# Performance work log

Hardware: AMD Instinct MI355X
Metric: run time of the kernel (lower is better)

The kernel has to match this reference:

```python
import jax, jax.numpy as jnp
import numpy as np

N_NODES = 100000
N_EDGES = 1000000
S = 64      # n_hidden_scalars
F = 64      # n_hidden_edge_feats
RBF = 16    # rbf_dim
V = 16      # n_vec_channels
IN_DIM = 2 * S + F + RBF  # 208, EdgeUpdate MLP input


def _layernorm(x, g, b):
    m = x.mean(-1, keepdims=True)
    var = ((x - m) ** 2).mean(-1, keepdims=True)
    return (x - m) / jnp.sqrt(var + 1e-5) * g + b


def _gvp(s, v, Wh, Wu, Ws, bs, sigmoid_gate):
    # s: [N, S]; v: [N, v_in, 3]
    vh = jnp.einsum('nvc,vh->nhc', v, Wh)          # [N, h, 3]
    vu = jnp.einsum('nhc,hu->nuc', vh, Wu)          # [N, v_out, 3]
    sh = jnp.sqrt(jnp.sum(vh * vh, axis=-1) + 1e-8)  # [N, h]
    s_out = jax.nn.silu(jnp.concatenate([s, sh], axis=-1) @ Ws + bs)
    vn = jnp.sqrt(jnp.sum(vu * vu, axis=-1, keepdims=True) + 1e-8)  # [N, v_out, 1]
    gate = jax.nn.sigmoid(vn) if sigmoid_gate else vn
    return s_out, gate * vu


def setup_inputs() -> dict:
    key = jax.random.key(0)
    ks = jax.random.split(key, 24)

    def nrm(k, shape, fan_in):
        return jax.random.normal(k, shape, dtype=jnp.float32) / np.sqrt(fan_in)

    inp = {
        'node_scalars': jax.random.normal(ks[0], (N_NODES, S), dtype=jnp.float32),
        'positions': jax.random.normal(ks[1], (N_NODES, 3), dtype=jnp.float32),
        'vectors': jax.random.normal(ks[2], (N_NODES, V, 3), dtype=jnp.float32),
        'edge_feats': jax.random.normal(ks[3], (N_EDGES, F), dtype=jnp.float32),
        'd': jax.random.uniform(ks[4], (N_EDGES, RBF), dtype=jnp.float32),
        'src_idx': jax.random.randint(ks[5], (N_EDGES,), 0, N_NODES, dtype=jnp.int32),
        'dst_idx': jax.random.randint(ks[6], (N_EDGES,), 0, N_NODES, dtype=jnp.int32),
        # EdgeUpdate MLP + LayerNorm params
        'W1': nrm(ks[7], (IN_DIM, F), IN_DIM), 'b1': jnp.zeros((F,), jnp.float32),
        'W2': nrm(ks[8], (F, F), F),           'b2': jnp.zeros((F,), jnp.float32),
        'ln_g': jnp.ones((F,), jnp.float32),   'ln_b': jnp.zeros((F,), jnp.float32),
        # GVP 0: s 64->64, v 16->16 (h=16), sigmoid vector gate
        'gvp0_Wh': nrm(ks[9], (V, V), V), 'gvp0_Wu': nrm(ks[10], (V, V), V),
        'gvp0_Ws': nrm(ks[11], (S + V, S), S + V), 'gvp0_bs': jnp.zeros((S,), jnp.float32),
        # GVP 1: same shapes
        'gvp1_Wh': nrm(ks[12], (V, V), V), 'gvp1_Wu': nrm(ks[13], (V, V), V),
        'gvp1_Ws': nrm(ks[14], (S + V, S), S + V), 'gvp1_bs': jnp.zeros((S,), jnp.float32),
        # GVP 2 (last): v 16->1, identity vector activation
        'gvp2_Wh': nrm(ks[15], (V, V), V), 'gvp2_Wu': nrm(ks[16], (V, 1), V),
        'gvp2_Ws': nrm(ks[17], (S + V, S), S + V), 'gvp2_bs': jnp.zeros((S,), jnp.float32),
    }
    return inp


def reference(node_scalars, positions, vectors, edge_feats, d, src_idx, dst_idx,
              W1, b1, W2, b2, ln_g, ln_b,
              gvp0_Wh, gvp0_Wu, gvp0_Ws, gvp0_bs,
              gvp1_Wh, gvp1_Wu, gvp1_Ws, gvp1_bs,
              gvp2_Wh, gvp2_Wu, gvp2_Ws, gvp2_bs):
    # ---- EdgeUpdate: gather-concat-MLP + residual + LayerNorm ----
    h = jnp.concatenate(
        [node_scalars[src_idx], node_scalars[dst_idx], edge_feats, d], axis=-1)  # [E, 208]
    h = jax.nn.silu(h @ W1 + b1)
    h = jax.nn.silu(h @ W2 + b2)
    edge_out = _layernorm(edge_feats + h, ln_g, ln_b)  # [E, F]

    # ---- NodePositionUpdate: 3 stacked GVPs, last emits 1 vector channel ----
    s, v = node_scalars, vectors
    s, v = _gvp(s, v, gvp0_Wh, gvp0_Wu, gvp0_Ws, gvp0_bs, sigmoid_gate=True)
    s, v = _gvp(s, v, gvp1_Wh, gvp1_Wu, gvp1_Ws, gvp1_bs, sigmoid_gate=True)
    s, v = _gvp(s, v, gvp2_Wh, gvp2_Wu, gvp2_Ws, gvp2_bs, sigmoid_gate=False)  # v: [N,1,3]
    pos_out = positions + v[:, 0, :]  # [N, 3]

    return edge_out, pos_out
```

## Files before the change

kernel.cpp:

```cpp
#include <hip/hip_runtime.h>
#include <hip/hip_bf16.h>

#define N_NODES 100000
#define N_EDGES 1000000
#define S_DIM 64
#define F_DIM 64
#define RBF_DIM 16
#define V_CH 16

typedef __attribute__((ext_vector_type(4))) float f32x4;
typedef __attribute__((ext_vector_type(8))) short bf16x8;

#define NBLK 128
#define TPW 5
#define EDGE_GRID 3125

__device__ __forceinline__ float silu_f(float x) {
    return x * (1.0f / (1.0f + __expf(-x)));
}

__device__ __forceinline__ ushort f2bf(float x) {
    union { __hip_bfloat16 b; ushort u; } c;
    c.b = __float2bfloat16(x);
    return c.u;
}

__device__ __forceinline__ f32x4 ld4v(const float* p) {
    return *reinterpret_cast<const f32x4*>(p);
}

__device__ __forceinline__ bf16x8 pack8(f32x4 u, f32x4 v) {
    bf16x8 r;
    r[0] = (short)f2bf(u[0]); r[1] = (short)f2bf(u[1]);
    r[2] = (short)f2bf(u[2]); r[3] = (short)f2bf(u[3]);
    r[4] = (short)f2bf(v[0]); r[5] = (short)f2bf(v[1]);
    r[6] = (short)f2bf(v[2]); r[7] = (short)f2bf(v[3]);
    return r;
}

struct RawG { f32x4 v[8]; };

__global__ __launch_bounds__(256, 3) void edge_kernel(
    const float* __restrict__ ns, const float* __restrict__ ef,
    const float* __restrict__ dd, const int* __restrict__ src,
    const int* __restrict__ dst, const float* __restrict__ W1,
    const float* __restrict__ b1, const float* __restrict__ W2,
    const float* __restrict__ b2, const float* __restrict__ lng,
    const float* __restrict__ lnb, float* __restrict__ out)
{
    __shared__ __align__(16) ushort b1f[7][4][64][8];
    __shared__ __align__(16) ushort b2f[2][4][64][8];

    const int tid  = threadIdx.x;
    const int lane = tid & 63;
    const int wid  = tid >> 6;
    const int l15  = lane & 15;
    const int g    = lane >> 4;

    {
        const int fl   = tid & 63;
        const int fnn  = tid >> 6;
        const int fl15 = fl & 15;
        const int fg   = fl >> 4;
        const int col  = 16 * fnn + fl15;
        const int krow = fg << 3;
        #pragma unroll
        for (int kk = 0; kk < 7; ++kk) {
            const int k0 = 32 * kk + krow;
            bf16x8 w;
            #pragma unroll
            for (int j = 0; j < 8; ++j) {
                const int k = k0 + j;
                w[j] = (k < 208) ? (short)f2bf(W1[k * 64 + col]) : (short)0;
            }
            *reinterpret_cast<bf16x8*>(&b1f[kk][fnn][fl][0]) = w;
        }
        #pragma unroll
        for (int kk = 0; kk < 2; ++kk) {
            bf16x8 w;
            #pragma unroll
            for (int j = 0; j < 8; ++j) {
                const int delta = 16 * (2 * kk + (j >> 2)) + 4 * fg + (j & 3);
                w[j] = (short)f2bf(W2[delta * 64 + col]);
            }
            *reinterpret_cast<bf16x8*>(&b2f[kk][fnn][fl][0]) = w;
        }
    }
    __syncthreads();

    f32x4 b1q[4], b2q[4];
    #pragma unroll
    for (int nn = 0; nn < 4; ++nn) {
        b1q[nn] = ld4v(b1 + 16 * nn + 4 * g);
        b2q[nn] = ld4v(b2 + 16 * nn + 4 * g);
    }

    const int wtile0 = (blockIdx.x * 4 + wid) * TPW;

    int sis[TPW], dis[TPW];
    #pragma unroll
    for (int t = 0; t < TPW; ++t) {
        const int erow = (wtile0 + t) * 16 + l15;
        sis[t] = src[erow];
        dis[t] = dst[erow];
    }

    auto load_gather = [&](RawG& r, int t) {
        const float* ps = ns + (size_t)sis[t] * 64 + 8 * g;
        const float* pd = ns + (size_t)dis[t] * 64 + 8 * g;
        r.v[0] = ld4v(ps);      r.v[1] = ld4v(ps + 4);
        r.v[2] = ld4v(ps + 32); r.v[3] = ld4v(ps + 36);
        r.v[4] = ld4v(pd);      r.v[5] = ld4v(pd + 4);
        r.v[6] = ld4v(pd + 32); r.v[7] = ld4v(pd + 36);
    };

    RawG r;
    load_gather(r, 0);

    #pragma unroll
    for (int t = 0; t < TPW; ++t) {
        const int ebase = (wtile0 + t) * 16;
        const int erow  = ebase + l15;

        const float* pe = ef + (size_t)erow * 64;
        const float* pr = dd + (size_t)erow * 16;
        const f32x4 e0 = ld4v(pe + 8 * g), e1 = ld4v(pe + 8 * g + 4);
        const f32x4 e2 = ld4v(pe + 32 + 8 * g), e3 = ld4v(pe + 32 + 8 * g + 4);
        f32x4 r0 = {0.f,0.f,0.f,0.f}, r1 = {0.f,0.f,0.f,0.f};
        if (g < 2) { r0 = ld4v(pr + 8 * g); r1 = ld4v(pr + 8 * g + 4); }
        f32x4 efq[4];
        #pragma unroll
        for (int nn = 0; nn < 4; ++nn) efq[nn] = ld4v(pe + 16 * nn + 4 * g);

        bf16x8 a0 = pack8(r.v[0], r.v[1]);
        bf16x8 a1 = pack8(r.v[2], r.v[3]);
        bf16x8 a2f = pack8(r.v[4], r.v[5]);
        bf16x8 a3 = pack8(r.v[6], r.v[7]);
        bf16x8 a4 = pack8(e0, e1);
        bf16x8 a5 = pack8(e2, e3);
        bf16x8 a6 = pack8(r0, r1);

        if (t < TPW - 1) load_gather(r, t + 1);

        f32x4 acc[4];
        #pragma unroll
        for (int nn = 0; nn < 4; ++nn) acc[nn] = (f32x4){0.f, 0.f, 0.f, 0.f};
        #pragma unroll
        for (int nn = 0; nn < 4; ++nn) {
            acc[nn] = __builtin_amdgcn_mfma_f32_16x16x32_bf16(*reinterpret_cast<const bf16x8*>(&b1f[0][nn][lane][0]), a0, acc[nn], 0, 0, 0);
            acc[nn] = __builtin_amdgcn_mfma_f32_16x16x32_bf16(*reinterpret_cast<const bf16x8*>(&b1f[1][nn][lane][0]), a1, acc[nn], 0, 0, 0);
            acc[nn] = __builtin_amdgcn_mfma_f32_16x16x32_bf16(*reinterpret_cast<const bf16x8*>(&b1f[2][nn][lane][0]), a2f, acc[nn], 0, 0, 0);
            acc[nn] = __builtin_amdgcn_mfma_f32_16x16x32_bf16(*reinterpret_cast<const bf16x8*>(&b1f[3][nn][lane][0]), a3, acc[nn], 0, 0, 0);
            acc[nn] = __builtin_amdgcn_mfma_f32_16x16x32_bf16(*reinterpret_cast<const bf16x8*>(&b1f[4][nn][lane][0]), a4, acc[nn], 0, 0, 0);
            acc[nn] = __builtin_amdgcn_mfma_f32_16x16x32_bf16(*reinterpret_cast<const bf16x8*>(&b1f[5][nn][lane][0]), a5, acc[nn], 0, 0, 0);
            acc[nn] = __builtin_amdgcn_mfma_f32_16x16x32_bf16(*reinterpret_cast<const bf16x8*>(&b1f[6][nn][lane][0]), a6, acc[nn], 0, 0, 0);
        }

        f32x4 sil[4];
        #pragma unroll
        for (int nn = 0; nn < 4; ++nn) {
            #pragma unroll
            for (int rr = 0; rr < 4; ++rr)
                sil[nn][rr] = silu_f(acc[nn][rr] + b1q[nn][rr]);
        }
        bf16x8 q0, q1;
        #pragma unroll
        for (int j = 0; j < 8; ++j) {
            q0[j] = (short)f2bf(sil[j >> 2][j & 3]);
            q1[j] = (short)f2bf(sil[2 + (j >> 2)][j & 3]);
        }

        f32x4 acc2[4];
        #pragma unroll
        for (int nn = 0; nn < 4; ++nn) acc2[nn] = (f32x4){0.f, 0.f, 0.f, 0.f};
        #pragma unroll
        for (int nn = 0; nn < 4; ++nn) {
            acc2[nn] = __builtin_amdgcn_mfma_f32_16x16x32_bf16(*reinterpret_cast<const bf16x8*>(&b2f[0][nn][lane][0]), q0, acc2[nn], 0, 0, 0);
            acc2[nn] = __builtin_amdgcn_mfma_f32_16x16x32_bf16(*reinterpret_cast<const bf16x8*>(&b2f[1][nn][lane][0]), q1, acc2[nn], 0, 0, 0);
        }

        f32x4 x[4];
        float s = 0.f;
        #pragma unroll
        for (int nn = 0; nn < 4; ++nn) {
            #pragma unroll
            for (int rr = 0; rr < 4; ++rr) {
                x[nn][rr] = silu_f(acc2[nn][rr] + b2q[nn][rr]) + efq[nn][rr];
                s += x[nn][rr];
            }
        }
        s += __shfl_xor(s, 16);
        s += __shfl_xor(s, 32);
        const float mean = s * (1.0f / 64.0f);

        float v = 0.f;
        #pragma unroll
        for (int nn = 0; nn < 4; ++nn) {
            #pragma unroll
            for (int rr = 0; rr < 4; ++rr) {
                const float dx = x[nn][rr] - mean;
                v += dx * dx;
            }
        }
        v += __shfl_xor(v, 16);
        v += __shfl_xor(v, 32);
        const float rsd = rsqrtf(v * (1.0f / 64.0f) + 1e-5f);

        float* obase = out + (size_t)erow * 64;
        #pragma unroll
        for (int nn = 0; nn < 4; ++nn) {
            const f32x4 lg = ld4v(lng + 16 * nn + 4 * g);
            const f32x4 lb = ld4v(lnb + 16 * nn + 4 * g);
            f32x4 o;
            #pragma unroll
            for (int rr = 0; rr < 4; ++rr)
                o[rr] = (x[nn][rr] - mean) * rsd * lg[rr] + lb[rr];
            *reinterpret_cast<f32x4*>(obase + 16 * nn + 4 * g) = o;
        }
    }
}

template <int UOUT, bool SIG>
__device__ __forceinline__ void gvp_step(
    float* __restrict__ s, float* __restrict__ vv,
    const float* __restrict__ Wh, const float* __restrict__ Wu,
    const float* __restrict__ Ws, const float* __restrict__ bs,
    float (*cat)[NBLK], const int tid)
{
    #pragma unroll
    for (int j = 0; j < 64; ++j) cat[j][tid] = s[j];

    float vu[UOUT * 3];
    #pragma unroll
    for (int i = 0; i < UOUT * 3; ++i) vu[i] = 0.0f;

    for (int h = 0; h < V_CH; ++h) {
        float t0 = 0.0f, t1 = 0.0f, t2 = 0.0f;
        #pragma unroll
        for (int vi = 0; vi < V_CH; ++vi) {
            const float wv = Wh[vi * V_CH + h];
            t0 = fmaf(vv[vi * 3 + 0], wv, t0);
            t1 = fmaf(vv[vi * 3 + 1], wv, t1);
            t2 = fmaf(vv[vi * 3 + 2], wv, t2);
        }
        cat[64 + h][tid] = sqrtf(t0 * t0 + t1 * t1 + t2 * t2 + 1e-8f);
        #pragma unroll
        for (int u = 0; u < UOUT; ++u) {
            const float wu = Wu[h * UOUT + u];
            vu[u * 3 + 0] = fmaf(t0, wu, vu[u * 3 + 0]);
            vu[u * 3 + 1] = fmaf(t1, wu, vu[u * 3 + 1]);
            vu[u * 3 + 2] = fmaf(t2, wu, vu[u * 3 + 2]);
        }
    }

    float acc[64];
    #pragma unroll
    for (int j = 0; j < 64; ++j) acc[j] = bs[j];
    #pragma unroll 2
    for (int k = 0; k < 64 + V_CH; ++k) {
        const float hk = cat[k][tid];
        const float* w = Ws + (size_t)k * 64;
        #pragma unroll
        for (int j = 0; j < 64; ++j) acc[j] = fmaf(hk, w[j], acc[j]);
    }
    #pragma unroll
    for (int j = 0; j < 64; ++j) s[j] = silu_f(acc[j]);

    #pragma unroll
    for (int u = 0; u < UOUT; ++u) {
        const float a = vu[u * 3 + 0];
        const float b = vu[u * 3 + 1];
        const float c = vu[u * 3 + 2];
        const float vn = sqrtf(a * a + b * b + c * c + 1e-8f);
        const float gt = SIG ? (1.0f / (1.0f + __expf(-vn))) : vn;
        vv[u * 3 + 0] = gt * a;
        vv[u * 3 + 1] = gt * b;
        vv[u * 3 + 2] = gt * c;
    }
}

__global__ __launch_bounds__(NBLK, 2) void node_kernel(
    const float* __restrict__ ns, const float* __restrict__ pos,
    const float* __restrict__ vec,
    const float* __restrict__ Wh0, const float* __restrict__ Wu0,
    const float* __restrict__ Ws0, const float* __restrict__ bs0,
    const float* __restrict__ Wh1, const float* __restrict__ Wu1,
    const float* __restrict__ Ws1, const float* __restrict__ bs1,
    const float* __restrict__ Wh2, const float* __restrict__ Wu2,
    const float* __restrict__ Ws2, const float* __restrict__ bs2,
    float* __restrict__ outpos)
{
    __shared__ float cat[64 + V_CH][NBLK];
    const int tid = threadIdx.x;
    const int n = blockIdx.x * NBLK + tid;
    const bool active = (n < N_NODES);
    const int nc = active ? n : 0;

    float s[64];
    {
        const float* p = ns + (size_t)nc * S_DIM;
        #pragma unroll
        for (int i = 0; i < 16; ++i) {
            float4 v4 = *reinterpret_cast<const float4*>(p + 4 * i);
            s[4 * i] = v4.x; s[4 * i + 1] = v4.y; s[4 * i + 2] = v4.z; s[4 * i + 3] = v4.w;
        }
    }
    float vv[48];
    {
        const float* p = vec + (size_t)nc * (V_CH * 3);
        #pragma unroll
        for (int i = 0; i < 12; ++i) {
            float4 v4 = *reinterpret_cast<const float4*>(p + 4 * i);
            vv[4 * i] = v4.x; vv[4 * i + 1] = v4.y; vv[4 * i + 2] = v4.z; vv[4 * i + 3] = v4.w;
        }
    }

    gvp_step<V_CH, true>(s, vv, Wh0, Wu0, Ws0, bs0, cat, tid);
    gvp_step<V_CH, true>(s, vv, Wh1, Wu1, Ws1, bs1, cat, tid);
    gvp_step<1, false>(s, vv, Wh2, Wu2, Ws2, bs2, cat, tid);

    if (active) {
        outpos[(size_t)n * 3 + 0] = pos[(size_t)n * 3 + 0] + vv[0];
        outpos[(size_t)n * 3 + 1] = pos[(size_t)n * 3 + 1] + vv[1];
        outpos[(size_t)n * 3 + 2] = pos[(size_t)n * 3 + 2] + vv[2];
    }
}

extern "C" void kernel_launch(void* const* d_in, const int* in_sizes, int n_in,
                              void* d_out, int out_size, void* d_ws, size_t ws_size,
                              hipStream_t stream) {
    const float* ns  = (const float*)d_in[0];
    const float* pos = (const float*)d_in[1];
    const float* vec = (const float*)d_in[2];
    const float* ef  = (const float*)d_in[3];
    const float* dd  = (const float*)d_in[4];
    const int*   src = (const int*)d_in[5];
    const int*   dst = (const int*)d_in[6];
    const float* W1  = (const float*)d_in[7];
    const float* b1  = (const float*)d_in[8];
    const float* W2  = (const float*)d_in[9];
    const float* b2  = (const float*)d_in[10];
    const float* lng = (const float*)d_in[11];
    const float* lnb = (const float*)d_in[12];
    const float* Wh0 = (const float*)d_in[13];
    const float* Wu0 = (const float*)d_in[14];
    const float* Ws0 = (const float*)d_in[15];
    const float* bs0 = (const float*)d_in[16];
    const float* Wh1 = (const float*)d_in[17];
    const float* Wu1 = (const float*)d_in[18];
    const float* Ws1 = (const float*)d_in[19];
    const float* bs1 = (const float*)d_in[20];
    const float* Wh2 = (const float*)d_in[21];
    const float* Wu2 = (const float*)d_in[22];
    const float* Ws2 = (const float*)d_in[23];
    const float* bs2 = (const float*)d_in[24];

    float* out     = (float*)d_out;
    float* out_pos = out + (size_t)N_EDGES * F_DIM;

    edge_kernel<<<EDGE_GRID, 256, 0, stream>>>(
        ns, ef, dd, src, dst, W1, b1, W2, b2, lng, lnb, out);
    node_kernel<<<(N_NODES + NBLK - 1) / NBLK, NBLK, 0, stream>>>(
        ns, pos, vec, Wh0, Wu0, Ws0, bs0, Wh1, Wu1, Ws1, bs1, Wh2, Wu2, Ws2, bs2, out_pos);
}
```

Measured before the change: 317.1 us.

## Pre-convert MLP weights once and read MFMA operands from global cache instead of LDS

Moves the W1/W2 fp32-to-bf16 fragment packing out of every edge block into a single prep kernel that writes a workspace buffer. The edge kernel then drops its shared-memory weight tiles and the __syncthreads, and loads MFMA B-fragments straight from global memory (L1/L2-resident) on each tile. An empty asm barrier on the pointer stops the compiler from hoisting all those loads into registers. This removes per-block conversion work and LDS usage, which may raise occupancy, at the cost of repeated global/cache reads of the weights and an extra kernel launch.

```diff
diff --git a/kernel.cpp b/kernel.cpp
--- a/kernel.cpp
+++ b/kernel.cpp
@@ -14,6 +14,9 @@
 #define NBLK 128
 #define TPW 5
 #define EDGE_GRID 3125
+
+#define W2OFF 14336
+#define WBUF_USHORTS 18432
 
 __device__ __forceinline__ float silu_f(float x) {
     return x * (1.0f / (1.0f + __expf(-x)));
@@ -40,53 +43,52 @@
 
 struct RawG { f32x4 v[8]; };
 
+__global__ void prep_weights(const float* __restrict__ W1, const float* __restrict__ W2,
+                             ushort* __restrict__ wbuf)
+{
+    const int tid  = threadIdx.x;
+    const int fl   = tid & 63;
+    const int fnn  = tid >> 6;
+    const int fl15 = fl & 15;
+    const int fg   = fl >> 4;
+    const int col  = 16 * fnn + fl15;
+    const int krow = fg << 3;
+    #pragma unroll
+    for (int kk = 0; kk < 7; ++kk) {
+        const int k0 = 32 * kk + krow;
+        bf16x8 w;
+        #pragma unroll
+        for (int j = 0; j < 8; ++j) {
+            const int k = k0 + j;
+            w[j] = (k < 208) ? (short)f2bf(W1[k * 64 + col]) : (short)0;
+        }
+        *reinterpret_cast<bf16x8*>(wbuf + ((size_t)(kk * 4 + fnn) * 64 + fl) * 8) = w;
+    }
+    #pragma unroll
+    for (int kk = 0; kk < 2; ++kk) {
+        bf16x8 w;
+        #pragma unroll
+        for (int j = 0; j < 8; ++j) {
+            const int delta = 16 * (2 * kk + (j >> 2)) + 4 * fg + (j & 3);
+            w[j] = (short)f2bf(W2[delta * 64 + col]);
+        }
+        *reinterpret_cast<bf16x8*>(wbuf + W2OFF + ((size_t)(kk * 4 + fnn) * 64 + fl) * 8) = w;
+    }
+}
+
 __global__ __launch_bounds__(256, 3) void edge_kernel(
     const float* __restrict__ ns, const float* __restrict__ ef,
     const float* __restrict__ dd, const int* __restrict__ src,
-    const int* __restrict__ dst, const float* __restrict__ W1,
-    const float* __restrict__ b1, const float* __restrict__ W2,
-    const float* __restrict__ b2, const float* __restrict__ lng,
-    const float* __restrict__ lnb, float* __restrict__ out)
+    const int* __restrict__ dst, const ushort* __restrict__ wbuf,
+    const float* __restrict__ b1, const float* __restrict__ b2,
+    const float* __restrict__ lng, const float* __restrict__ lnb,
+    float* __restrict__ out)
 {
-    __shared__ __align__(16) ushort b1f[7][4][64][8];
-    __shared__ __align__(16) ushort b2f[2][4][64][8];
-
     const int tid  = threadIdx.x;
     const int lane = tid & 63;
     const int wid  = tid >> 6;
     const int l15  = lane & 15;
     const int g    = lane >> 4;
-
-    {
-        const int fl   = tid & 63;
-        const int fnn  = tid >> 6;
-        const int fl15 = fl & 15;
-        const int fg   = fl >> 4;
-        const int col  = 16 * fnn + fl15;
-        const int krow = fg << 3;
-        #pragma unroll
-        for (int kk = 0; kk < 7; ++kk) {
-            const int k0 = 32 * kk + krow;
-            bf16x8 w;
-            #pragma unroll
-            for (int j = 0; j < 8; ++j) {
-                const int k = k0 + j;
-                w[j] = (k < 208) ? (short)f2bf(W1[k * 64 + col]) : (short)0;
-            }
-            *reinterpret_cast<bf16x8*>(&b1f[kk][fnn][fl][0]) = w;
-        }
-        #pragma unroll
-        for (int kk = 0; kk < 2; ++kk) {
-            bf16x8 w;
-            #pragma unroll
-            for (int j = 0; j < 8; ++j) {
-                const int delta = 16 * (2 * kk + (j >> 2)) + 4 * fg + (j & 3);
-                w[j] = (short)f2bf(W2[delta * 64 + col]);
-            }
-            *reinterpret_cast<bf16x8*>(&b2f[kk][fnn][fl][0]) = w;
-        }
-    }
-    __syncthreads();
 
     f32x4 b1q[4], b2q[4];
     #pragma unroll
@@ -119,15 +121,17 @@
 
     #pragma unroll
     for (int t = 0; t < TPW; ++t) {
-        const int ebase = (wtile0 + t) * 16;
-        const int erow  = ebase + l15;
+        const int erow = (wtile0 + t) * 16 + l15;
+
+        const ushort* wb = wbuf;
+        asm volatile("" : "+v"(wb));
 
         const float* pe = ef + (size_t)erow * 64;
-        const float* pr = dd + (size_t)erow * 16;
+        const float* pr = dd + (size_t)erow * 16 + 8 * g;
         const f32x4 e0 = ld4v(pe + 8 * g), e1 = ld4v(pe + 8 * g + 4);
         const f32x4 e2 = ld4v(pe + 32 + 8 * g), e3 = ld4v(pe + 32 + 8 * g + 4);
         f32x4 r0 = {0.f,0.f,0.f,0.f}, r1 = {0.f,0.f,0.f,0.f};
-        if (g < 2) { r0 = ld4v(pr + 8 * g); r1 = ld4v(pr + 8 * g + 4); }
+        if (g < 2) { r0 = ld4v(pr); r1 = ld4v(pr + 4); }
         f32x4 efq[4];
         #pragma unroll
         for (int nn = 0; nn < 4; ++nn) efq[nn] = ld4v(pe + 16 * nn + 4 * g);
@@ -142,18 +146,20 @@
 
         if (t < TPW - 1) load_gather(r, t + 1);
 
+        #define W1F(kk) (*reinterpret_cast<const bf16x8*>(wb + ((size_t)((kk) * 4 + nn) * 64 + lane) * 8))
+        #define W2F(kk) (*reinterpret_cast<const bf16x8*>(wb + W2OFF + ((size_t)((kk) * 4 + nn) * 64 + lane) * 8))
         f32x4 acc[4];
         #pragma unroll
         for (int nn = 0; nn < 4; ++nn) acc[nn] = (f32x4){0.f, 0.f, 0.f, 0.f};
         #pragma unroll
         for (int nn = 0; nn < 4; ++nn) {
-            acc[nn] = __builtin_amdgcn_mfma_f32_16x16x32_bf16(*reinterpret_cast<const bf16x8*>(&b1f[0][nn][lane][0]), a0, acc[nn], 0, 0, 0);
-            acc[nn] = __builtin_amdgcn_mfma_f32_16x16x32_bf16(*reinterpret_cast<const bf16x8*>(&b1f[1][nn][lane][0]), a1, acc[nn], 0, 0, 0);
-            acc[nn] = __builtin_amdgcn_mfma_f32_16x16x32_bf16(*reinterpret_cast<const bf16x8*>(&b1f[2][nn][lane][0]), a2f, acc[nn], 0, 0, 0);
-            acc[nn] = __builtin_amdgcn_mfma_f32_16x16x32_bf16(*reinterpret_cast<const bf16x8*>(&b1f[3][nn][lane][0]), a3, acc[nn], 0, 0, 0);
-            acc[nn] = __builtin_amdgcn_mfma_f32_16x16x32_bf16(*reinterpret_cast<const bf16x8*>(&b1f[4][nn][lane][0]), a4, acc[nn], 0, 0, 0);
-            acc[nn] = __builtin_amdgcn_mfma_f32_16x16x32_bf16(*reinterpret_cast<const bf16x8*>(&b1f[5][nn][lane][0]), a5, acc[nn], 0, 0, 0);
-            acc[nn] = __builtin_amdgcn_mfma_f32_16x16x32_bf16(*reinterpret_cast<const bf16x8*>(&b1f[6][nn][lane][0]), a6, acc[nn], 0, 0, 0);
+            acc[nn] = __builtin_amdgcn_mfma_f32_16x16x32_bf16(W1F(0), a0, acc[nn], 0, 0, 0);
+            acc[nn] = __builtin_amdgcn_mfma_f32_16x16x32_bf16(W1F(1), a1, acc[nn], 0, 0, 0);
+            acc[nn] = __builtin_amdgcn_mfma_f32_16x16x32_bf16(W1F(2), a2f, acc[nn], 0, 0, 0);
+            acc[nn] = __builtin_amdgcn_mfma_f32_16x16x32_bf16(W1F(3), a3, acc[nn], 0, 0, 0);
+            acc[nn] = __builtin_amdgcn_mfma_f32_16x16x32_bf16(W1F(4), a4, acc[nn], 0, 0, 0);
+            acc[nn] = __builtin_amdgcn_mfma_f32_16x16x32_bf16(W1F(5), a5, acc[nn], 0, 0, 0);
+            acc[nn] = __builtin_amdgcn_mfma_f32_16x16x32_bf16(W1F(6), a6, acc[nn], 0, 0, 0);
         }
 
         f32x4 sil[4];
@@ -175,9 +181,11 @@
         for (int nn = 0; nn < 4; ++nn) acc2[nn] = (f32x4){0.f, 0.f, 0.f, 0.f};
         #pragma unroll
         for (int nn = 0; nn < 4; ++nn) {
-            acc2[nn] = __builtin_amdgcn_mfma_f32_16x16x32_bf16(*reinterpret_cast<const bf16x8*>(&b2f[0][nn][lane][0]), q0, acc2[nn], 0, 0, 0);
-            acc2[nn] = __builtin_amdgcn_mfma_f32_16x16x32_bf16(*reinterpret_cast<const bf16x8*>(&b2f[1][nn][lane][0]), q1, acc2[nn], 0, 0, 0);
-        }
+            acc2[nn] = __builtin_amdgcn_mfma_f32_16x16x32_bf16(W2F(0), q0, acc2[nn], 0, 0, 0);
+            acc2[nn] = __builtin_amdgcn_mfma_f32_16x16x32_bf16(W2F(1), q1, acc2[nn], 0, 0, 0);
+        }
+        #undef W1F
+        #undef W2F
 
         f32x4 x[4];
         float s = 0.f;
@@ -355,11 +363,13 @@
     const float* Ws2 = (const float*)d_in[23];
     const float* bs2 = (const float*)d_in[24];
 
-    float* out     = (float*)d_out;
-    float* out_pos = out + (size_t)N_EDGES * F_DIM;
-
+    float*  out     = (float*)d_out;
+    float*  out_pos = out + (size_t)N_EDGES * F_DIM;
+    ushort* wbuf    = (ushort*)d_ws;
+
+    prep_weights<<<1, 256, 0, stream>>>(W1, W2, wbuf);
     edge_kernel<<<EDGE_GRID, 256, 0, stream>>>(
-        ns, ef, dd, src, dst, W1, b1, W2, b2, lng, lnb, out);
+        ns, ef, dd, src, dst, wbuf, b1, b2, lng, lnb, out);
     node_kernel<<<(N_NODES + NBLK - 1) / NBLK, NBLK, 0, stream>>>(
         ns, pos, vec, Wh0, Wu0, Ws0, bs0, Wh1, Wu1, Ws1, bs1, Wh2, Wu2, Ws2, bs2, out_pos);
 }
```

New measurement: 402.2 us. 1.27x slower.
